# Optimization experiments

Measured on AMD Instinct MI355X. Metric: run time of the kernel, lower is better.

## Reference

```python
import jax, jax.numpy as jnp
import numpy as np

K = 7          # involution kernel size
G = 16         # groups = channels // group_channels = 256 // 16
BN_EPS = 1e-3  # Keras BatchNormalization default epsilon


def setup_inputs() -> dict:
    key = jax.random.key(0)
    ks = jax.random.split(key, 6)
    B, H, W, C = 4, 56, 56, 256
    Cr = C // 4                      # reduction_ratio = 4
    x = jax.random.normal(ks[0], (B, H, W, C), dtype=jnp.float32)
    w_reduce = jax.random.normal(ks[1], (C, Cr), dtype=jnp.float32) * (1.0 / np.sqrt(C))
    gamma = jnp.ones((Cr,), dtype=jnp.float32)
    beta = jnp.zeros((Cr,), dtype=jnp.float32)
    mean = jax.random.normal(ks[2], (Cr,), dtype=jnp.float32) * 0.1
    var = jax.random.uniform(ks[3], (Cr,), dtype=jnp.float32) + 0.5
    w_span = jax.random.normal(ks[4], (Cr, K * K * G), dtype=jnp.float32) * (1.0 / np.sqrt(Cr))
    b_span = jnp.zeros((K * K * G,), dtype=jnp.float32)
    return {"x": x, "w_reduce": w_reduce, "gamma": gamma, "beta": beta,
            "mean": mean, "var": var, "w_span": w_span, "b_span": b_span}


def reference(x, w_reduce, gamma, beta, mean, var, w_span, b_span):
    B, H, W, C = x.shape
    Cg = C // G  # channels per group
    # kernel generation branch: 1x1 conv -> BN (inference) -> ReLU -> 1x1 conv
    r = jnp.einsum('bhwc,cd->bhwd', x, w_reduce)
    r = jax.nn.relu((r - mean) * (gamma / jnp.sqrt(var + BN_EPS)) + beta)
    kgen = jnp.einsum('bhwd,de->bhwe', r, w_span) + b_span      # (B,H,W,K*K*G)
    kgen = kgen.reshape(B, H, W, G, K * K)
    # im2col with SAME padding (stride=1, pad (K-1)//2 symmetric), depth order (kh, kw, C)
    p = (K - 1) // 2
    xp = jnp.pad(x, ((0, 0), (p, p), (p, p), (0, 0)))
    patches = jnp.stack([xp[:, i:i + H, j:j + W, :]
                         for i in range(K) for j in range(K)], axis=3)  # (B,H,W,K*K,C)
    patches = patches.reshape(B, H, W, K * K, G, Cg)
    # per-pixel, per-group weighted reduction over the K*K window
    out = jnp.einsum('bhwgk,bhwkgc->bhwgc', kgen, patches)
    return out.reshape(B, H, W, C)
```

## Files before the change

### kernel.cpp

```cpp
#include <hip/hip_runtime.h>
#include <stdint.h>

#define B_   4
#define H_   56
#define W_   56
#define C_   256
#define CR   64
#define G_   16
#define CG   16
#define KS   7
#define KK   49
#define PADR 3
#define NPX  (B_*H_*W_)

typedef __attribute__((ext_vector_type(8))) short bf16x8;
typedef __attribute__((ext_vector_type(4))) float f32x4;

__device__ __forceinline__ uint32_t f2bf(float f) {
    uint32_t x = __float_as_uint(f);
    return (x + 0x7fffu + ((x >> 16) & 1u)) >> 16;
}
__device__ __forceinline__ float bf2f(uint32_t u) {
    return __uint_as_float(u << 16);
}

__global__ __launch_bounds__(256) void k0_prepack(
        const float* __restrict__ wr, const float* __restrict__ wspan,
        const float* __restrict__ gamma, const float* __restrict__ beta,
        const float* __restrict__ mean, const float* __restrict__ var,
        uint16_t* __restrict__ wrp, uint16_t* __restrict__ wpp,
        float* __restrict__ scale, float* __restrict__ shift) {
    int idx = blockIdx.x * 256 + threadIdx.x;
    {
        int j = idx & 7, lane = (idx >> 3) & 63, nb = (idx >> 9) & 3,
            kb = (idx >> 11) & 1, g = idx >> 12;
        int k = kb * 32 + (lane >> 4) * 8 + j;
        int n = nb * 16 + (lane & 15);
        float v = (n < KK) ? wspan[k * (KK * G_) + g * KK + n] : 0.f;
        wpp[idx] = (uint16_t)f2bf(v);
    }
    if (idx < 16384) {
        int j = idx & 7, lane = (idx >> 3) & 63, nb = (idx >> 9) & 3, kb = idx >> 11;
        int k = kb * 32 + (lane >> 4) * 8 + j;
        int n = nb * 16 + (lane & 15);
        wrp[idx] = (uint16_t)f2bf(wr[k * CR + n]);
    }
    if (idx < CR) {
        float s = gamma[idx] * rsqrtf(var[idx] + 1e-3f);
        scale[idx] = s;
        shift[idx] = beta[idx] - mean[idx] * s;
    }
}

__global__ __launch_bounds__(64) void k1_reduce(
        const float* __restrict__ x, const uint16_t* __restrict__ wrp,
        const float* __restrict__ scale, const float* __restrict__ shift,
        uint16_t* __restrict__ r) {
    int lane = threadIdx.x;
    int mt = blockIdx.x;
    int pix = mt * 16 + (lane & 15);
    const float* xrow = x + (size_t)pix * C_ + (lane >> 4) * 8;
    f32x4 acc[4] = {{0,0,0,0},{0,0,0,0},{0,0,0,0},{0,0,0,0}};
    for (int kb = 0; kb < 8; ++kb) {
        float4 a0 = *(const float4*)(xrow + kb * 32);
        float4 a1 = *(const float4*)(xrow + kb * 32 + 4);
        bf16x8 af;
        af[0] = (short)f2bf(a0.x); af[1] = (short)f2bf(a0.y);
        af[2] = (short)f2bf(a0.z); af[3] = (short)f2bf(a0.w);
        af[4] = (short)f2bf(a1.x); af[5] = (short)f2bf(a1.y);
        af[6] = (short)f2bf(a1.z); af[7] = (short)f2bf(a1.w);
        const uint16_t* wb = wrp + kb * 2048 + lane * 8;
        #pragma unroll
        for (int nb = 0; nb < 4; ++nb) {
            bf16x8 bf_ = *(const bf16x8*)(wb + nb * 512);
            acc[nb] = __builtin_amdgcn_mfma_f32_16x16x32_bf16(af, bf_, acc[nb], 0, 0, 0);
        }
    }
    int rq = (lane >> 4) * 4;
    #pragma unroll
    for (int nb = 0; nb < 4; ++nb) {
        int d = nb * 16 + (lane & 15);
        float s = scale[d], sh = shift[d];
        #pragma unroll
        for (int rg = 0; rg < 4; ++rg) {
            float v = fmaf(acc[nb][rg], s, sh);
            v = v > 0.f ? v : 0.f;
            r[(size_t)(mt * 16 + rq + rg) * CR + d] = (uint16_t)f2bf(v);
        }
    }
}

#define TS    14
#define HS    20
#define XP    20
#define ROWS  404

__global__ __launch_bounds__(256, 3) void k2_involution(
        const float* __restrict__ x, const uint16_t* __restrict__ r,
        const uint16_t* __restrict__ wpp, const float* __restrict__ bspan,
        float* __restrict__ out) {
    __shared__ float    xs[HS * ROWS];
    __shared__ uint16_t kg[208 * KK];

    int tid  = threadIdx.x;
    int tile = blockIdx.x, g = blockIdx.y, b = blockIdx.z;
    int ty0 = (tile >> 2) * TS, tx0 = (tile & 3) * TS;

    #pragma unroll
    for (int pass = 0; pass < 2; ++pass) {
        int i = tid + pass * 256;
        if (i < HS * HS) {
            int py = i / HS, px = i % HS;
            int gy = ty0 + py - PADR, gx = tx0 + px - PADR;
            float4 v0, v1, v2, v3;
            if (gy >= 0 && gy < H_ && gx >= 0 && gx < W_) {
                const float* xp = x + (((size_t)(b * H_ + gy)) * W_ + gx) * C_ + g * CG;
                v0 = *(const float4*)(xp + 0);
                v1 = *(const float4*)(xp + 4);
                v2 = *(const float4*)(xp + 8);
                v3 = *(const float4*)(xp + 12);
            } else {
                v0 = v1 = v2 = v3 = make_float4(0.f, 0.f, 0.f, 0.f);
            }
            float* dst = xs + py * ROWS + px * XP;
            *(float4*)(dst + 0)  = v0;
            *(float4*)(dst + 4)  = v1;
            *(float4*)(dst + 8)  = v2;
            *(float4*)(dst + 12) = v3;
        }
    }

    int lane = tid & 63, w = tid >> 6;
    bf16x8 bfr[2][4];
    const uint16_t* wb = wpp + g * 4096 + lane * 8;
    #pragma unroll
    for (int kb = 0; kb < 2; ++kb)
        #pragma unroll
        for (int nb = 0; nb < 4; ++nb)
            bfr[kb][nb] = *(const bf16x8*)(wb + kb * 2048 + nb * 512);
    float bias[4];
    #pragma unroll
    for (int nb = 0; nb < 4; ++nb) {
        int n = nb * 16 + (lane & 15);
        bias[nb] = (n < KK) ? bspan[g * KK + n] : 0.f;
    }
    for (int mi = 0; mi < 4; ++mi) {
        int mt = mi * 4 + w;
        if (mt < 13) {
            int m  = mt * 16 + (lane & 15);
            int mm = m < 196 ? m : 195;
            int ly = mm / TS, lx = mm % TS;
            size_t pix = ((size_t)(b * H_ + ty0 + ly)) * W_ + (tx0 + lx);
            const uint16_t* rp = r + pix * CR + (lane >> 4) * 8;
            bf16x8 a0 = *(const bf16x8*)(rp);
            bf16x8 a1 = *(const bf16x8*)(rp + 32);
            f32x4 acc[4];
            #pragma unroll
            for (int nb = 0; nb < 4; ++nb)
                acc[nb] = (f32x4){bias[nb], bias[nb], bias[nb], bias[nb]};
            #pragma unroll
            for (int nb = 0; nb < 4; ++nb) {
                acc[nb] = __builtin_amdgcn_mfma_f32_16x16x32_bf16(a0, bfr[0][nb], acc[nb], 0, 0, 0);
                acc[nb] = __builtin_amdgcn_mfma_f32_16x16x32_bf16(a1, bfr[1][nb], acc[nb], 0, 0, 0);
            }
            #pragma unroll
            for (int nb = 0; nb < 4; ++nb) {
                int n = nb * 16 + (lane & 15);
                if (n < KK) {
                    int row = mt * 16 + (lane >> 4) * 4;
                    #pragma unroll
                    for (int rg = 0; rg < 4; ++rg)
                        kg[(row + rg) * KK + n] = (uint16_t)f2bf(acc[nb][rg]);
                }
            }
        }
    }
    __syncthreads();

    if (tid < 98) {
        int ty  = tid / 7;
        int tx2 = (tid % 7) * 2;
        float accL[CG], accR[CG];
        #pragma unroll
        for (int c = 0; c < CG; ++c) { accL[c] = 0.f; accR[c] = 0.f; }
        const uint16_t* kgL = kg + (ty * TS + tx2) * KK;
        const uint16_t* kgR = kgL + KK;
        for (int kh = 0; kh < KS; ++kh) {
            const float* xrow = xs + (ty + kh) * ROWS + tx2 * XP;
            #pragma unroll
            for (int p = 0; p < 8; ++p) {
                float kvL = 0.f, kvR = 0.f;
                if (p < 7) kvL = bf2f(kgL[kh * 7 + p]);
                if (p > 0) kvR = bf2f(kgR[kh * 7 + p - 1]);
                const float* xp = xrow + p * XP;
                #pragma unroll
                for (int c4 = 0; c4 < 4; ++c4) {
                    float4 xv = *(const float4*)(xp + c4 * 4);
                    if (p < 7) {
                        accL[c4*4+0] = fmaf(kvL, xv.x, accL[c4*4+0]);
                        accL[c4*4+1] = fmaf(kvL, xv.y, accL[c4*4+1]);
                        accL[c4*4+2] = fmaf(kvL, xv.z, accL[c4*4+2]);
                        accL[c4*4+3] = fmaf(kvL, xv.w, accL[c4*4+3]);
                    }
                    if (p > 0) {
                        accR[c4*4+0] = fmaf(kvR, xv.x, accR[c4*4+0]);
                        accR[c4*4+1] = fmaf(kvR, xv.y, accR[c4*4+1]);
                        accR[c4*4+2] = fmaf(kvR, xv.z, accR[c4*4+2]);
                        accR[c4*4+3] = fmaf(kvR, xv.w, accR[c4*4+3]);
                    }
                }
            }
        }
        size_t pixL = ((size_t)(b * H_ + ty0 + ty)) * W_ + (tx0 + tx2);
        float* opL = out + pixL * C_ + g * CG;
        float* opR = opL + C_;
        *(float4*)(opL + 0)  = make_float4(accL[0],  accL[1],  accL[2],  accL[3]);
        *(float4*)(opL + 4)  = make_float4(accL[4],  accL[5],  accL[6],  accL[7]);
        *(float4*)(opL + 8)  = make_float4(accL[8],  accL[9],  accL[10], accL[11]);
        *(float4*)(opL + 12) = make_float4(accL[12], accL[13], accL[14], accL[15]);
        *(float4*)(opR + 0)  = make_float4(accR[0],  accR[1],  accR[2],  accR[3]);
        *(float4*)(opR + 4)  = make_float4(accR[4],  accR[5],  accR[6],  accR[7]);
        *(float4*)(opR + 8)  = make_float4(accR[8],  accR[9],  accR[10], accR[11]);
        *(float4*)(opR + 12) = make_float4(accR[12], accR[13], accR[14], accR[15]);
    }
}

extern "C" void kernel_launch(void* const* d_in, const int* in_sizes, int n_in,
                              void* d_out, int out_size, void* d_ws, size_t ws_size,
                              hipStream_t stream) {
    const float* x        = (const float*)d_in[0];
    const float* w_reduce = (const float*)d_in[1];
    const float* gamma    = (const float*)d_in[2];
    const float* beta     = (const float*)d_in[3];
    const float* mean     = (const float*)d_in[4];
    const float* var      = (const float*)d_in[5];
    const float* w_span   = (const float*)d_in[6];
    const float* b_span   = (const float*)d_in[7];
    float* out = (float*)d_out;

    uint8_t* ws = (uint8_t*)d_ws;
    uint16_t* r_ws  = (uint16_t*)(ws + 0);
    uint16_t* wrp   = (uint16_t*)(ws + 1605632);
    uint16_t* wpp   = (uint16_t*)(ws + 1638400);
    float*    scale = (float*)   (ws + 1769472);
    float*    shift = (float*)   (ws + 1769728);

    hipLaunchKernelGGL(k0_prepack, dim3(256), dim3(256), 0, stream,
                       w_reduce, w_span, gamma, beta, mean, var,
                       wrp, wpp, scale, shift);
    hipLaunchKernelGGL(k1_reduce, dim3(NPX / 16), dim3(64), 0, stream,
                       x, wrp, scale, shift, r_ws);
    hipLaunchKernelGGL(k2_involution, dim3(16, 16, B_), dim3(256), 0, stream,
                       x, r_ws, wpp, b_span, out);
}
```

Baseline: 105.7 us.

## Store involution tile in bf16 LDS, split channels across threads, use packed FMA

Stores the input halo tile in shared memory as bf16 instead of fp32, and pads the per-pixel kernel rows to 56 entries so 16-byte vector loads work. The weighted-reduction stage now uses 196 threads, each covering half the channels of a pixel pair, and preloads its kernel weights into registers. Accumulation uses packed two-wide FMAs, and the reduce kernel uses the bf16x2 conversion intrinsic. This cuts LDS footprint and traffic and raises thread utilisation, but x is now rounded to bf16 in the involution product, which adds precision loss.

```diff
diff --git a/kernel.cpp b/kernel.cpp
--- a/kernel.cpp
+++ b/kernel.cpp
@@ -1,4 +1,5 @@
 #include <hip/hip_runtime.h>
+#include <hip/hip_bf16.h>
 #include <stdint.h>
 
 #define B_   4
@@ -15,14 +16,21 @@
 
 typedef __attribute__((ext_vector_type(8))) short bf16x8;
 typedef __attribute__((ext_vector_type(4))) float f32x4;
+typedef __attribute__((ext_vector_type(2))) float f32x2;
 
 __device__ __forceinline__ uint32_t f2bf(float f) {
     uint32_t x = __float_as_uint(f);
     return (x + 0x7fffu + ((x >> 16) & 1u)) >> 16;
 }
-__device__ __forceinline__ float bf2f(uint32_t u) {
-    return __uint_as_float(u << 16);
-}
+__device__ __forceinline__ uint32_t pkbf(float a, float b) {
+    union { __hip_bfloat162 h; uint32_t u; } c;
+    c.h = __float22bfloat162_rn(make_float2(a, b));
+    return c.u;
+}
+__device__ __forceinline__ float blo(uint32_t w) { return __uint_as_float(w << 16); }
+__device__ __forceinline__ float bhi(uint32_t w) { return __uint_as_float(w & 0xffff0000u); }
+
+union U4V { uint4 u; bf16x8 v; };
 
 __global__ __launch_bounds__(256) void k0_prepack(
         const float* __restrict__ wr, const float* __restrict__ wspan,
@@ -64,16 +72,14 @@
     for (int kb = 0; kb < 8; ++kb) {
         float4 a0 = *(const float4*)(xrow + kb * 32);
         float4 a1 = *(const float4*)(xrow + kb * 32 + 4);
-        bf16x8 af;
-        af[0] = (short)f2bf(a0.x); af[1] = (short)f2bf(a0.y);
-        af[2] = (short)f2bf(a0.z); af[3] = (short)f2bf(a0.w);
-        af[4] = (short)f2bf(a1.x); af[5] = (short)f2bf(a1.y);
-        af[6] = (short)f2bf(a1.z); af[7] = (short)f2bf(a1.w);
+        U4V af;
+        af.u = make_uint4(pkbf(a0.x, a0.y), pkbf(a0.z, a0.w),
+                          pkbf(a1.x, a1.y), pkbf(a1.z, a1.w));
         const uint16_t* wb = wrp + kb * 2048 + lane * 8;
         #pragma unroll
         for (int nb = 0; nb < 4; ++nb) {
             bf16x8 bf_ = *(const bf16x8*)(wb + nb * 512);
-            acc[nb] = __builtin_amdgcn_mfma_f32_16x16x32_bf16(af, bf_, acc[nb], 0, 0, 0);
+            acc[nb] = __builtin_amdgcn_mfma_f32_16x16x32_bf16(af.v, bf_, acc[nb], 0, 0, 0);
         }
     }
     int rq = (lane >> 4) * 4;
@@ -90,17 +96,18 @@
     }
 }
 
-#define TS    14
-#define HS    20
-#define XP    20
-#define ROWS  404
+#define TS   14
+#define HS   20
+#define XSW  24
+#define XROW (21*XSW)
+#define KGW  56
 
 __global__ __launch_bounds__(256, 3) void k2_involution(
         const float* __restrict__ x, const uint16_t* __restrict__ r,
         const uint16_t* __restrict__ wpp, const float* __restrict__ bspan,
         float* __restrict__ out) {
-    __shared__ float    xs[HS * ROWS];
-    __shared__ uint16_t kg[208 * KK];
+    __shared__ __align__(16) uint16_t xs[HS * XROW];
+    __shared__ __align__(16) uint16_t kg[208 * KGW];
 
     int tid  = threadIdx.x;
     int tile = blockIdx.x, g = blockIdx.y, b = blockIdx.z;
@@ -112,21 +119,21 @@
         if (i < HS * HS) {
             int py = i / HS, px = i % HS;
             int gy = ty0 + py - PADR, gx = tx0 + px - PADR;
-            float4 v0, v1, v2, v3;
+            uint4 wA = make_uint4(0, 0, 0, 0), wB = wA;
             if (gy >= 0 && gy < H_ && gx >= 0 && gx < W_) {
                 const float* xp = x + (((size_t)(b * H_ + gy)) * W_ + gx) * C_ + g * CG;
-                v0 = *(const float4*)(xp + 0);
-                v1 = *(const float4*)(xp + 4);
-                v2 = *(const float4*)(xp + 8);
-                v3 = *(const float4*)(xp + 12);
-            } else {
-                v0 = v1 = v2 = v3 = make_float4(0.f, 0.f, 0.f, 0.f);
-            }
-            float* dst = xs + py * ROWS + px * XP;
-            *(float4*)(dst + 0)  = v0;
-            *(float4*)(dst + 4)  = v1;
-            *(float4*)(dst + 8)  = v2;
-            *(float4*)(dst + 12) = v3;
+                float4 v0 = *(const float4*)(xp + 0);
+                float4 v1 = *(const float4*)(xp + 4);
+                float4 v2 = *(const float4*)(xp + 8);
+                float4 v3 = *(const float4*)(xp + 12);
+                wA = make_uint4(pkbf(v0.x, v0.y), pkbf(v0.z, v0.w),
+                                pkbf(v1.x, v1.y), pkbf(v1.z, v1.w));
+                wB = make_uint4(pkbf(v2.x, v2.y), pkbf(v2.z, v2.w),
+                                pkbf(v3.x, v3.y), pkbf(v3.z, v3.w));
+            }
+            uint16_t* dst = xs + py * XROW + px * XSW;
+            *(uint4*)(dst + 0) = wA;
+            *(uint4*)(dst + 8) = wB;
         }
     }
 
@@ -170,58 +177,60 @@
                     int row = mt * 16 + (lane >> 4) * 4;
                     #pragma unroll
                     for (int rg = 0; rg < 4; ++rg)
-                        kg[(row + rg) * KK + n] = (uint16_t)f2bf(acc[nb][rg]);
+                        kg[(row + rg) * KGW + n] = (uint16_t)f2bf(acc[nb][rg]);
                 }
             }
         }
     }
     __syncthreads();
 
-    if (tid < 98) {
-        int ty  = tid / 7;
-        int tx2 = (tid % 7) * 2;
-        float accL[CG], accR[CG];
-        #pragma unroll
-        for (int c = 0; c < CG; ++c) { accL[c] = 0.f; accR[c] = 0.f; }
-        const uint16_t* kgL = kg + (ty * TS + tx2) * KK;
-        const uint16_t* kgR = kgL + KK;
+    if (tid < 196) {
+        int p = tid >> 1, h = tid & 1;
+        int ty = p / 7, tx = (p % 7) * 2;
+        int rowL = ty * TS + tx;
+
+        uint32_t kwL[28], kwR[28];
+        #pragma unroll
+        for (int t = 0; t < 7; ++t) {
+            uint4 a = *(const uint4*)(kg + rowL * KGW + t * 8);
+            uint4 c = *(const uint4*)(kg + (rowL + 1) * KGW + t * 8);
+            kwL[t*4+0] = a.x; kwL[t*4+1] = a.y; kwL[t*4+2] = a.z; kwL[t*4+3] = a.w;
+            kwR[t*4+0] = c.x; kwR[t*4+1] = c.y; kwR[t*4+2] = c.z; kwR[t*4+3] = c.w;
+        }
+
+        f32x2 accL[4] = {{0,0},{0,0},{0,0},{0,0}};
+        f32x2 accR[4] = {{0,0},{0,0},{0,0},{0,0}};
+        #pragma unroll
         for (int kh = 0; kh < KS; ++kh) {
-            const float* xrow = xs + (ty + kh) * ROWS + tx2 * XP;
-            #pragma unroll
-            for (int p = 0; p < 8; ++p) {
+            const uint16_t* xrow = xs + (ty + kh) * XROW + tx * XSW + h * 8;
+            #pragma unroll
+            for (int j = 0; j < 8; ++j) {
+                uint4 xw = *(const uint4*)(xrow + j * XSW);
                 float kvL = 0.f, kvR = 0.f;
-                if (p < 7) kvL = bf2f(kgL[kh * 7 + p]);
-                if (p > 0) kvR = bf2f(kgR[kh * 7 + p - 1]);
-                const float* xp = xrow + p * XP;
-                #pragma unroll
-                for (int c4 = 0; c4 < 4; ++c4) {
-                    float4 xv = *(const float4*)(xp + c4 * 4);
-                    if (p < 7) {
-                        accL[c4*4+0] = fmaf(kvL, xv.x, accL[c4*4+0]);
-                        accL[c4*4+1] = fmaf(kvL, xv.y, accL[c4*4+1]);
-                        accL[c4*4+2] = fmaf(kvL, xv.z, accL[c4*4+2]);
-                        accL[c4*4+3] = fmaf(kvL, xv.w, accL[c4*4+3]);
-                    }
-                    if (p > 0) {
-                        accR[c4*4+0] = fmaf(kvR, xv.x, accR[c4*4+0]);
-                        accR[c4*4+1] = fmaf(kvR, xv.y, accR[c4*4+1]);
-                        accR[c4*4+2] = fmaf(kvR, xv.z, accR[c4*4+2]);
-                        accR[c4*4+3] = fmaf(kvR, xv.w, accR[c4*4+3]);
-                    }
-                }
-            }
-        }
-        size_t pixL = ((size_t)(b * H_ + ty0 + ty)) * W_ + (tx0 + tx2);
-        float* opL = out + pixL * C_ + g * CG;
+                if (j < 7) { int t = kh * 7 + j;     kvL = (t & 1) ? bhi(kwL[t>>1]) : blo(kwL[t>>1]); }
+                if (j > 0) { int t = kh * 7 + j - 1; kvR = (t & 1) ? bhi(kwR[t>>1]) : blo(kwR[t>>1]); }
+                f32x2 kL = {kvL, kvL}, kR = {kvR, kvR};
+                f32x2 x0 = {blo(xw.x), bhi(xw.x)};
+                f32x2 x1 = {blo(xw.y), bhi(xw.y)};
+                f32x2 x2 = {blo(xw.z), bhi(xw.z)};
+                f32x2 x3 = {blo(xw.w), bhi(xw.w)};
+                accL[0] = __builtin_elementwise_fma(kL, x0, accL[0]);
+                accL[1] = __builtin_elementwise_fma(kL, x1, accL[1]);
+                accL[2] = __builtin_elementwise_fma(kL, x2, accL[2]);
+                accL[3] = __builtin_elementwise_fma(kL, x3, accL[3]);
+                accR[0] = __builtin_elementwise_fma(kR, x0, accR[0]);
+                accR[1] = __builtin_elementwise_fma(kR, x1, accR[1]);
+                accR[2] = __builtin_elementwise_fma(kR, x2, accR[2]);
+                accR[3] = __builtin_elementwise_fma(kR, x3, accR[3]);
+            }
+        }
+        size_t pixL = ((size_t)(b * H_ + ty0 + ty)) * W_ + (tx0 + tx);
+        float* opL = out + pixL * C_ + g * CG + h * 8;
         float* opR = opL + C_;
-        *(float4*)(opL + 0)  = make_float4(accL[0],  accL[1],  accL[2],  accL[3]);
-        *(float4*)(opL + 4)  = make_float4(accL[4],  accL[5],  accL[6],  accL[7]);
-        *(float4*)(opL + 8)  = make_float4(accL[8],  accL[9],  accL[10], accL[11]);
-        *(float4*)(opL + 12) = make_float4(accL[12], accL[13], accL[14], accL[15]);
-        *(float4*)(opR + 0)  = make_float4(accR[0],  accR[1],  accR[2],  accR[3]);
-        *(float4*)(opR + 4)  = make_float4(accR[4],  accR[5],  accR[6],  accR[7]);
-        *(float4*)(opR + 8)  = make_float4(accR[8],  accR[9],  accR[10], accR[11]);
-        *(float4*)(opR + 12) = make_float4(accR[12], accR[13], accR[14], accR[15]);
+        *(float4*)(opL + 0) = make_float4(accL[0].x, accL[0].y, accL[1].x, accL[1].y);
+        *(float4*)(opL + 4) = make_float4(accL[2].x, accL[2].y, accL[3].x, accL[3].y);
+        *(float4*)(opR + 0) = make_float4(accR[0].x, accR[0].y, accR[1].x, accR[1].y);
+        *(float4*)(opR + 4) = make_float4(accR[2].x, accR[2].y, accR[3].x, accR[3].y);
     }
 }
 
```

Measured after the change: 100.1 us. 1.06x faster.
